# Kernel tuning notes

Hardware: AMD Instinct MI355X
Metric: run time of the kernel (lower is better)

Reference implementation:

```python
import jax, jax.numpy as jnp
import numpy as np

B, QL, CTX, H = 1, 2048, 2048, 4096
NH, NKV, HD = 32, 8, 128


def rotate_half(x):
    x1, x2 = jnp.split(x, 2, axis=-1)
    return jnp.concatenate([-x2, x1], axis=-1)


def apply_rotary(x, cos, sin):
    # x: [B, h, S, HD]; cos/sin: [B, S, HD] -> broadcast over heads
    cos = cos[:, None, :, :]
    sin = sin[:, None, :, :]
    return x * cos + rotate_half(x) * sin


def setup_inputs() -> dict:
    key = jax.random.key(0)
    ks = jax.random.split(key, 8)
    s = 0.02
    return {
        "hidden_states": jax.random.normal(ks[0], (B, QL, H), jnp.float32),
        "target_hidden": jax.random.normal(ks[1], (B, CTX, H), jnp.float32),
        "cos": jax.random.uniform(ks[2], (B, CTX + QL, HD), jnp.float32),
        "sin": jax.random.uniform(ks[3], (B, CTX + QL, HD), jnp.float32),
        "Wq": jax.random.normal(ks[4], (NH * HD, H), jnp.float32) * s,
        "Wk": jax.random.normal(ks[5], (NKV * HD, H), jnp.float32) * s,
        "Wv": jax.random.normal(ks[6], (NKV * HD, H), jnp.float32) * s,
        "Wo": jax.random.normal(ks[7], (H, NH * HD), jnp.float32) * s,
    }


def reference(hidden_states, target_hidden, cos, sin, Wq, Wk, Wv, Wo):
    bsz, q_len, _ = hidden_states.shape
    ctx_len = target_hidden.shape[1]

    def proj(x, W, nh):  # [B,S,H] @ W.T -> [B,nh,S,HD]
        y = jnp.einsum("bsh,dh->bsd", x, W)
        return y.reshape(bsz, x.shape[1], nh, HD).transpose(0, 2, 1, 3)

    q = proj(hidden_states, Wq, NH)
    k_ctx = proj(target_hidden, Wk, NKV)
    v_ctx = proj(target_hidden, Wv, NKV)
    k_noise = proj(hidden_states, Wk, NKV)
    v_noise = proj(hidden_states, Wv, NKV)

    cos_n = cos[:, ctx_len:ctx_len + q_len]
    sin_n = sin[:, ctx_len:ctx_len + q_len]
    q = apply_rotary(q, cos_n, sin_n)
    k_noise = apply_rotary(k_noise, cos_n, sin_n)
    k_ctx = apply_rotary(k_ctx, cos[:, :ctx_len], sin[:, :ctx_len])

    k = jnp.concatenate([k_ctx, k_noise], axis=2)  # [B,NKV,CTX+QL,HD]
    v = jnp.concatenate([v_ctx, v_noise], axis=2)

    n_rep = NH // NKV
    k = jnp.repeat(k, n_rep, axis=1)  # repeat_interleave on head dim
    v = jnp.repeat(v, n_rep, axis=1)

    scale = 1.0 / jnp.sqrt(jnp.asarray(HD, q.dtype))
    scores = jnp.einsum("bhqd,bhkd->bhqk", q, k) * scale
    probs = jax.nn.softmax(scores, axis=-1)
    attn = jnp.einsum("bhqk,bhkd->bhqd", probs, v)
    attn = attn.transpose(0, 2, 1, 3).reshape(bsz, q_len, NH * HD)
    return jnp.einsum("bsd,hd->bsh", attn, Wo)
```

## Files before the change

### kernel.cpp

```cpp
#include <hip/hip_runtime.h>

typedef unsigned short u16;
typedef _Float16 f16;
typedef _Float16 f16x4 __attribute__((ext_vector_type(4)));
typedef _Float16 f16x8 __attribute__((ext_vector_type(8)));
typedef float f32x4 __attribute__((ext_vector_type(4)));

#define GLL16(gptr, lptr)                                                        \
  __builtin_amdgcn_global_load_lds(                                              \
      (const __attribute__((address_space(1))) void*)(gptr),                     \
      (__attribute__((address_space(3))) void*)(lptr), 16, 0, 0)

__global__ void cast_all_k(const float* __restrict__ h, const float* __restrict__ t,
                           const float* __restrict__ wq, const float* __restrict__ wk,
                           const float* __restrict__ wv, const float* __restrict__ wo,
                           f16* __restrict__ Xcat, f16* __restrict__ Wqb,
                           f16* __restrict__ Wkvb, f16* __restrict__ Wob) {
  long i = (long)blockIdx.x * 256 + threadIdx.x;
  const float* s; f16* d; long off;
  if (i < 2097152)        { s = h;  d = Xcat;            off = i; }
  else if (i < 4194304)   { s = t;  d = Xcat + 8388608;  off = i - 2097152; }
  else if (i < 8388608)   { s = wq; d = Wqb;             off = i - 4194304; }
  else if (i < 9437184)   { s = wk; d = Wkvb;            off = i - 8388608; }
  else if (i < 10485760)  { s = wv; d = Wkvb + 4194304;  off = i - 9437184; }
  else                    { s = wo; d = Wob;             off = i - 10485760; }
  float4 v = *(const float4*)(s + off * 4);
  f16x4 o;
  o.x = (f16)v.x; o.y = (f16)v.y; o.z = (f16)v.z; o.w = (f16)v.w;
  *(f16x4*)(d + off * 4) = o;
}

template <int MODE>
__global__ __launch_bounds__(512, 2) void gemm8k(
    const f16* __restrict__ Xcat, const f16* __restrict__ Wqb,
    const f16* __restrict__ Wkvb, const float* __restrict__ cosT,
    const float* __restrict__ sinT, f16* __restrict__ Qb, f16* __restrict__ Kb,
    f16* __restrict__ Vt, const f16* __restrict__ Ao,
    const f16* __restrict__ Wob, float* __restrict__ Cp, float qscale) {
  __shared__ __align__(16) f16 lds[65536];
  const int tid = threadIdx.x;
  const int w = tid >> 6, lane = tid & 63;
  const int quad = lane >> 4, l16 = lane & 15;
  const int wm = w >> 1, wn = w & 1;

  int b = (int)blockIdx.x;
  int l = ((b & 7) << 5) | (b >> 3);

  const f16 *A, *B;
  long tM, tN;
  int NT, kbeg;
  bool isQ = false, isV = false;
  float* Cz = nullptr;
  if (MODE == 0) {
    kbeg = 0; NT = 64;
    if (l < 128) {
      A = Xcat; B = Wqb; tM = (long)(l >> 4) * 256; tN = (long)(l & 15) * 256;
      isQ = true;
    } else {
      int l2 = l - 128;
      A = Xcat; B = Wkvb; tM = (long)(l2 >> 3) * 256; tN = (long)(l2 & 7) * 256;
      isV = (tN >= 1024);
    }
  } else {
    int z = l >> 7, r0 = l & 127;
    A = Ao; B = Wob; tM = (long)(r0 >> 4) * 256; tN = (long)(r0 & 15) * 256;
    kbeg = z * 2048; NT = 32; Cz = Cp + (long)z * 8388608;
  }

  const int sr8 = lane >> 3;
  const int cg = (lane & 7) ^ sr8;
  const f16* Ag = A + (tM + 16 * w + sr8) * 4096 + kbeg + cg * 8;
  const f16* Bg = B + (tN + 16 * w + sr8) * 4096 + kbeg + cg * 8;
  const int ldsw = w * 1024;

#define STAGE_A(hf, t, c)                                                      \
  do {                                                                         \
    const f16* g_ = Ag + (long)(t) * 64 + (long)(hf) * (128 * 4096);           \
    f16* d_ = &lds[(c) * 16384 + (hf) * 8192 + ldsw];                          \
    GLL16(g_, d_);                                                             \
    GLL16(g_ + 8 * 4096, d_ + 512);                                            \
  } while (0)
#define STAGE_B(hf, t, c)                                                      \
  do {                                                                         \
    const f16* g_ = Bg + (long)(t) * 64 + (long)(hf) * (128 * 4096);           \
    f16* d_ = &lds[32768 + (c) * 16384 + (hf) * 8192 + ldsw];                  \
    GLL16(g_, d_);                                                             \
    GLL16(g_ + 8 * 4096, d_ + 512);                                            \
  } while (0)

  const int rA = wm * 64 + l16;
  const int rB = wn * 128 + l16;
  const int sw = l16 & 7;
#define LDA(fr, mi, kk, c)                                                     \
  fr = *(const f16x8*)&lds[(c) * 16384 + (rA + (mi) * 16) * 64 +               \
                           (((kk) * 4 + quad) ^ sw) * 8]
#define LDB(fr, ni, kk, c)                                                     \
  fr = *(const f16x8*)&lds[32768 + (c) * 16384 + (rB + (ni) * 16) * 64 +       \
                           (((kk) * 4 + quad) ^ sw) * 8]

#define MFMA16 __builtin_amdgcn_mfma_f32_16x16x32_f16
#define BAR() __builtin_amdgcn_s_barrier()
#define WAITDS()                                                               \
  do {                                                                         \
    asm volatile("s_waitcnt lgkmcnt(0)" ::: "memory");                         \
    __builtin_amdgcn_sched_barrier(0);                                         \
  } while (0)

  f32x4 acc[4][8] = {};
  f16x8 af[2][2], bf0[4][2], bf1[4][2];

  STAGE_B(0, 0, 0); STAGE_B(1, 0, 0); STAGE_A(0, 0, 0); STAGE_A(1, 0, 0);
  STAGE_B(0, 1, 1); STAGE_B(1, 1, 1);
  asm volatile("s_waitcnt vmcnt(4)" ::: "memory");
  BAR();

#define TILE_STEP(t, c)                                                        \
  do {                                                                         \
                                       \
    LDA(af[0][0], 0, 0, c); LDA(af[0][1], 0, 1, c);                            \
    LDA(af[1][0], 1, 0, c); LDA(af[1][1], 1, 1, c);                            \
    LDB(bf0[0][0], 0, 0, c); LDB(bf0[0][1], 0, 1, c);                          \
    LDB(bf0[1][0], 1, 0, c); LDB(bf0[1][1], 1, 1, c);                          \
    LDB(bf0[2][0], 2, 0, c); LDB(bf0[2][1], 2, 1, c);                          \
    LDB(bf0[3][0], 3, 0, c); LDB(bf0[3][1], 3, 1, c);                          \
    if ((t) + 1 < NT) STAGE_A(0, (t) + 1, (c) ^ 1);                            \
    BAR(); WAITDS();                                                           \
    __builtin_amdgcn_s_setprio(1);                                             \
    _Pragma("unroll") for (int mi = 0; mi < 2; ++mi)                           \
        _Pragma("unroll") for (int ni = 0; ni < 4; ++ni) {                     \
      acc[mi][ni] = MFMA16(af[mi][0], bf0[ni][0], acc[mi][ni], 0, 0, 0);       \
      acc[mi][ni] = MFMA16(af[mi][1], bf0[ni][1], acc[mi][ni], 0, 0, 0);       \
    }                                                                          \
    __builtin_amdgcn_s_setprio(0);                                             \
    BAR();                                                                     \
                                       \
    LDB(bf1[0][0], 4, 0, c); LDB(bf1[0][1], 4, 1, c);                          \
    LDB(bf1[1][0], 5, 0, c); LDB(bf1[1][1], 5, 1, c);                          \
    LDB(bf1[2][0], 6, 0, c); LDB(bf1[2][1], 6, 1, c);                          \
    LDB(bf1[3][0], 7, 0, c); LDB(bf1[3][1], 7, 1, c);                          \
    if ((t) + 1 < NT) STAGE_A(1, (t) + 1, (c) ^ 1);                            \
    BAR(); WAITDS();                                                           \
    __builtin_amdgcn_s_setprio(1);                                             \
    _Pragma("unroll") for (int mi = 0; mi < 2; ++mi)                           \
        _Pragma("unroll") for (int ni = 0; ni < 4; ++ni) {                     \
      acc[mi][4 + ni] =                                                        \
          MFMA16(af[mi][0], bf1[ni][0], acc[mi][4 + ni], 0, 0, 0);             \
      acc[mi][4 + ni] =                                                        \
          MFMA16(af[mi][1], bf1[ni][1], acc[mi][4 + ni], 0, 0, 0);             \
    }                                                                          \
    __builtin_amdgcn_s_setprio(0);                                             \
    BAR();                                                                     \
                                       \
    LDA(af[0][0], 2, 0, c); LDA(af[0][1], 2, 1, c);                            \
    LDA(af[1][0], 3, 0, c); LDA(af[1][1], 3, 1, c);                            \
    if ((t) + 2 < NT) STAGE_B(0, (t) + 2, c);                                  \
    BAR(); WAITDS();                                                           \
    __builtin_amdgcn_s_setprio(1);                                             \
    _Pragma("unroll") for (int mi = 0; mi < 2; ++mi)                           \
        _Pragma("unroll") for (int ni = 0; ni < 4; ++ni) {                     \
      acc[2 + mi][ni] = MFMA16(af[mi][0], bf0[ni][0], acc[2 + mi][ni], 0, 0, 0);\
      acc[2 + mi][ni] = MFMA16(af[mi][1], bf0[ni][1], acc[2 + mi][ni], 0, 0, 0);\
    }                                                                          \
    __builtin_amdgcn_s_setprio(0);                                             \
    BAR();                                                                     \
      \
    if ((t) + 2 < NT) STAGE_B(1, (t) + 2, c);                                  \
    BAR();                                                                     \
    __builtin_amdgcn_s_setprio(1);                                             \
    _Pragma("unroll") for (int mi = 0; mi < 2; ++mi)                           \
        _Pragma("unroll") for (int ni = 0; ni < 4; ++ni) {                     \
      acc[2 + mi][4 + ni] =                                                    \
          MFMA16(af[mi][0], bf1[ni][0], acc[2 + mi][4 + ni], 0, 0, 0);         \
      acc[2 + mi][4 + ni] =                                                    \
          MFMA16(af[mi][1], bf1[ni][1], acc[2 + mi][4 + ni], 0, 0, 0);         \
    }                                                                          \
    __builtin_amdgcn_s_setprio(0);                                             \
    if ((t) + 2 < NT)                                                          \
      asm volatile("s_waitcnt vmcnt(4)" ::: "memory");                         \
    else                                                                       \
      asm volatile("s_waitcnt vmcnt(0)" ::: "memory");                         \
    BAR();                                                                     \
  } while (0)

  for (int t = 0; t < NT; t += 2) {
    TILE_STEP(t, 0);
    TILE_STEP(t + 1, 1);
  }

  if (MODE == 1) {
#pragma unroll
    for (int mi = 0; mi < 4; ++mi)
#pragma unroll
      for (int ni = 0; ni < 8; ++ni)
#pragma unroll
        for (int r = 0; r < 4; ++r) {
          long row = tM + wm * 64 + mi * 16 + quad * 4 + r;
          long col = tN + wn * 128 + ni * 16 + l16;
          Cz[row * 4096 + col] = acc[mi][ni][r];
        }
  } else if (isV) {
    const int kvh = (int)((tN - 1024) >> 7) + wn;
#pragma unroll
    for (int mi = 0; mi < 4; ++mi) {
      int key0 = ((int)tM + wm * 64 + mi * 16 + quad * 4) ^ 2048;
#pragma unroll
      for (int ni = 0; ni < 8; ++ni) {
        int d = ni * 16 + l16;
        f16x4 pk;
#pragma unroll
        for (int r = 0; r < 4; ++r) pk[r] = (f16)acc[mi][ni][r];
        *(f16x4*)&Vt[((long)kvh * 128 + d) * 4096 + key0] = pk;
      }
    }
  } else {
    const float sc = isQ ? qscale : 1.0f;
    const int h = (int)(tN >> 7) + wn;
#pragma unroll
    for (int mi = 0; mi < 4; ++mi)
#pragma unroll
      for (int r = 0; r < 4; ++r) {
        int rg = (int)tM + wm * 64 + mi * 16 + quad * 4 + r;
        int pos = isQ ? (2048 + rg) : (rg ^ 2048);
        const float* cp = cosT + (long)pos * 128;
        const float* sp = sinT + (long)pos * 128;
        f16* orow = isQ ? Qb + ((long)h * 2048 + rg) * 128
                        : Kb + ((long)h * 4096 + pos) * 128;
#pragma unroll
        for (int ni = 0; ni < 4; ++ni) {
          int d = ni * 16 + l16;
          float x0 = acc[mi][ni][r], x1 = acc[mi][ni + 4][r];
          orow[d] = (f16)((x0 * cp[d] - x1 * sp[d]) * sc);
          orow[d + 64] = (f16)((x1 * cp[d + 64] + x0 * sp[d + 64]) * sc);
        }
      }
  }
#undef TILE_STEP
#undef STAGE_A
#undef STAGE_B
#undef LDA
#undef LDB
#undef WAITDS
#undef BAR
#undef MFMA16
}

__global__ __launch_bounds__(256, 2) void flash_k(const f16* __restrict__ Qb,
                                                  const f16* __restrict__ Kb,
                                                  const f16* __restrict__ Vt,
                                                  f16* __restrict__ Ob) {
  __shared__ __align__(16) f16 Ks[2][64 * 128];
  __shared__ __align__(16) f16 Vs[2][128 * 64];
  __shared__ __align__(16) f16 Ps[4][32 * 64];
  const int tid = threadIdx.x;
  const int w = tid >> 6, lane = tid & 63;
  const int quad = lane >> 4, l16 = lane & 15;
  const int b = blockIdx.x;
  const int kvh = b & 7;
  const int j = b >> 3;
  const int h = kvh * 4 + (j >> 4);
  const int q0 = (j & 15) * 128;

  f16x8 qf[2][4];
#pragma unroll
  for (int mi = 0; mi < 2; ++mi) {
    const f16* qrow = Qb + ((long)h * 2048 + q0 + w * 32 + mi * 16 + l16) * 128 + quad * 8;
#pragma unroll
    for (int kc = 0; kc < 4; ++kc) qf[mi][kc] = *(const f16x8*)(qrow + kc * 32);
  }

  f32x4 of[2][8] = {};
  float lsum[2] = {0.f, 0.f};
  const f16* Kg = Kb + (long)kvh * 4096 * 128;
  const f16* Vg = Vt + (long)kvh * 128 * 4096;
  f16* PsW = &Ps[w][0];
  const int psw = l16 & 7;

  const int krow = (lane >> 4);
  const int kslot = lane & 15;
  const int vrow = (lane >> 3);
  const int vslot = lane & 7;
  const int vgc = vslot ^ (vrow & 7);

#define FBAR() __builtin_amdgcn_s_barrier()
#define STAGE_K(kt_, c_)                                                       \
  do {                                                                         \
    _Pragma("unroll") for (int it = 0; it < 4; ++it) {                         \
      int row = w * 16 + it * 4 + krow;                                        \
      int gc = kslot ^ (it * 4 + krow);                                        \
      GLL16(Kg + (long)((kt_)*64 + row) * 128 + gc * 8,                        \
            &Ks[c_][(w * 16 + it * 4) * 128]);                                 \
    }                                                                          \
  } while (0)
#define STAGE_V(kt_, c_)                                                       \
  do {                                                                         \
    _Pragma("unroll") for (int it = 0; it < 4; ++it) {                         \
      int row = w * 32 + it * 8 + vrow;                                        \
      GLL16(Vg + (long)row * 4096 + (kt_)*64 + vgc * 8,                        \
            &Vs[c_][(w * 32 + it * 8) * 64]);                                  \
    }                                                                          \
  } while (0)

#define QKT(dst, c_)                                                           \
  do {                                                                         \
    _Pragma("unroll") for (int nt = 0; nt < 4; ++nt) {                         \
      f16x8 ak[4];                                                             \
      _Pragma("unroll") for (int kc = 0; kc < 4; ++kc) {                       \
        int slot = (kc * 4 + quad) ^ l16;                                      \
        ak[kc] = *(const f16x8*)&Ks[c_][(nt * 16 + l16) * 128 + slot * 8];     \
      }                                                                        \
      _Pragma("unroll") for (int mi = 0; mi < 2; ++mi)                         \
          _Pragma("unroll") for (int kc = 0; kc < 4; ++kc)                     \
        dst[mi][nt] = __builtin_amdgcn_mfma_f32_16x16x32_f16(                  \
            ak[kc], qf[mi][kc], dst[mi][nt], 0, 0, 0);                         \
    }                                                                          \
  } while (0)

#define EXPP(src)                                                              \
  do {                                                                         \
    _Pragma("unroll") for (int mi = 0; mi < 2; ++mi)                           \
        _Pragma("unroll") for (int nt = 0; nt < 4; ++nt) {                     \
      f16x4 pk;                                                                \
      _Pragma("unroll") for (int r = 0; r < 4; ++r) {                          \
        float pv = __builtin_amdgcn_exp2f(src[mi][nt][r]);                     \
        lsum[mi] += pv;                                                        \
        pk[r] = (f16)pv;                                                       \
      }                                                                        \
      *(f16x4*)&PsW[(mi * 16 + l16) * 64 +                                     \
                    (((nt * 2 + (quad >> 1)) ^ psw) << 3) + ((quad & 1) << 2)] \
          = pk;                                                                \
    }                                                                          \
  } while (0)

#define PVACC(vb_)                                                             \
  do {                                                                         \
    _Pragma("unroll") for (int kc2 = 0; kc2 < 2; ++kc2) {                      \
      f16x8 bp[2];                                                             \
      _Pragma("unroll") for (int mi = 0; mi < 2; ++mi)                         \
        bp[mi] = *(const f16x8*)&PsW[(mi * 16 + l16) * 64 +                    \
                                     (((kc2 * 4 + quad) ^ psw) << 3)];         \
      _Pragma("unroll") for (int dt = 0; dt < 8; ++dt) {                       \
        int slot = (kc2 * 4 + quad) ^ (l16 & 7);                               \
        f16x8 av = *(const f16x8*)&Vs[vb_][(dt * 16 + l16) * 64 + slot * 8];   \
        _Pragma("unroll") for (int mi = 0; mi < 2; ++mi)                       \
          of[mi][dt] = __builtin_amdgcn_mfma_f32_16x16x32_f16(                 \
              av, bp[mi], of[mi][dt], 0, 0, 0);                                \
      }                                                                        \
    }                                                                          \
  } while (0)

#define ZEROS(s_)                                                              \
  do {                                                                         \
    _Pragma("unroll") for (int mi = 0; mi < 2; ++mi)                           \
        _Pragma("unroll") for (int nt = 0; nt < 4; ++nt)                       \
            s_[mi][nt] = f32x4{0.f, 0.f, 0.f, 0.f};                            \
  } while (0)

#define ITER(kt_, c_, sPrev, sCur)                                             \
  do {                                                                         \
    asm volatile("s_waitcnt vmcnt(4)" ::: "memory");         \
    FBAR();                                                                    \
    __builtin_amdgcn_sched_barrier(0);                                         \
    ZEROS(sCur);                                                               \
    __builtin_amdgcn_s_setprio(1);                                             \
    QKT(sCur, c_);                                                             \
    EXPP(sPrev);                                                               \
    PVACC((c_) ^ 1);                                                           \
    __builtin_amdgcn_s_setprio(0);                                             \
    FBAR();                                                                    \
    if ((kt_) < 63) {                                                          \
      STAGE_K((kt_) + 1, (c_) ^ 1);                                            \
      STAGE_V((kt_) + 1, (c_) ^ 1);                                            \
    }                                                                          \
  } while (0)

  f32x4 sA[2][4], sB[2][4];

  STAGE_K(0, 0); STAGE_V(0, 0);
  STAGE_K(1, 1); STAGE_V(1, 1);
  asm volatile("s_waitcnt vmcnt(8)" ::: "memory");
  FBAR();
  __builtin_amdgcn_sched_barrier(0);
  ZEROS(sA);
  __builtin_amdgcn_s_setprio(1);
  QKT(sA, 0);
  __builtin_amdgcn_s_setprio(0);

  for (int kt = 1; kt < 63; kt += 2) {
    ITER(kt, 1, sA, sB);
    ITER(kt + 1, 0, sB, sA);
  }
  ITER(63, 1, sA, sB);

  EXPP(sB);
  asm volatile("s_waitcnt vmcnt(0)" ::: "memory");
  FBAR();
  PVACC(1);

#undef ITER
#undef ZEROS
#undef STAGE_K
#undef STAGE_V
#undef QKT
#undef EXPP
#undef PVACC
#undef FBAR

#pragma unroll
  for (int mi = 0; mi < 2; ++mi) {
    float v = lsum[mi];
    v += __shfl_xor(v, 16, 64);
    v += __shfl_xor(v, 32, 64);
    float inv = 1.0f / v;
    long q = q0 + w * 32 + mi * 16 + l16;
#pragma unroll
    for (int dt = 0; dt < 8; ++dt) {
      f16x4 o4;
#pragma unroll
      for (int r = 0; r < 4; ++r) o4[r] = (f16)(of[mi][dt][r] * inv);
      *(f16x4*)&Ob[q * 4096 + h * 128 + dt * 16 + quad * 4] = o4;
    }
  }
}

__global__ void reduce2_k(const float* __restrict__ p, float* __restrict__ out) {
  long i = ((long)blockIdx.x * 256 + threadIdx.x) * 4;
  float4 a = *(const float4*)(p + i);
  float4 b = *(const float4*)(p + 8388608 + i);
  a.x += b.x; a.y += b.y; a.z += b.z; a.w += b.w;
  *(float4*)(out + i) = a;
}

extern "C" void kernel_launch(void* const* d_in, const int* in_sizes, int n_in,
                              void* d_out, int out_size, void* d_ws, size_t ws_size,
                              hipStream_t stream) {
  (void)in_sizes; (void)n_in; (void)out_size; (void)ws_size;
  const float* hidden = (const float*)d_in[0];
  const float* target = (const float*)d_in[1];
  const float* cosT = (const float*)d_in[2];
  const float* sinT = (const float*)d_in[3];
  const float* Wq = (const float*)d_in[4];
  const float* Wk = (const float*)d_in[5];
  const float* Wv = (const float*)d_in[6];
  const float* Wo = (const float*)d_in[7];
  float* out = (float*)d_out;

  char* p = (char*)d_ws;
  auto alloc = [&](size_t bytes) {
    char* r = p;
    p += (bytes + 255) & ~(size_t)255;
    return r;
  };
  f16* Xcat = (f16*)alloc(4096ull * 4096 * 2);
  f16* Wqb  = (f16*)alloc(4096ull * 4096 * 2);
  f16* Wkvb = (f16*)alloc(2048ull * 4096 * 2);
  f16* Wob  = (f16*)alloc(4096ull * 4096 * 2);
  f16* Qb   = (f16*)alloc(32ull * 2048 * 128 * 2);
  f16* Kb   = (f16*)alloc(8ull * 4096 * 128 * 2);
  f16* Vt   = (f16*)alloc(8ull * 128 * 4096 * 2);
  f16* Ao   = (f16*)alloc(2048ull * 4096 * 2);
  float* Pp = (float*)d_ws;

  cast_all_k<<<57344, 256, 0, stream>>>(hidden, target, Wq, Wk, Wv, Wo,
                                        Xcat, Wqb, Wkvb, Wob);

  const float QSC = (float)(0.08838834764831845 * 1.4426950408889634);
  gemm8k<0><<<256, 512, 0, stream>>>(Xcat, Wqb, Wkvb, cosT, sinT, Qb, Kb, Vt,
                                     nullptr, nullptr, nullptr, QSC);

  flash_k<<<512, 256, 0, stream>>>(Qb, Kb, Vt, Ao);

  gemm8k<1><<<256, 512, 0, stream>>>(nullptr, nullptr, nullptr, nullptr, nullptr,
                                     nullptr, nullptr, nullptr, Ao, Wob, Pp, 0.f);
  reduce2_k<<<8192, 256, 0, stream>>>(Pp, out);
}
```

Baseline: 607.1 us.

## Split K and V staging into separate phases of the attention pipeline

Restructures the flash-attention inner loop so K and V tiles are prefetched at separate points. Each iteration now has two barrier phases: the first issues the next K tile and runs the PV accumulate, the second issues the V tile and runs QK^T and exp. The goal is to spread global-to-LDS traffic across the iteration and shorten waits on a combined K+V load. In exchange there are twice as many barriers per iteration and a longer hand-written prologue and epilogue that must keep the vmcnt counts and buffer indices correct.

```diff
diff --git a/kernel.cpp b/kernel.cpp
--- a/kernel.cpp
+++ b/kernel.cpp
@@ -282,6 +282,8 @@
   const int vgc = vslot ^ (vrow & 7);
 
 #define FBAR() __builtin_amdgcn_s_barrier()
+#define SCHED0() __builtin_amdgcn_sched_barrier(0)
+#define VMC(n) asm volatile("s_waitcnt vmcnt(" #n ")" ::: "memory")
 #define STAGE_K(kt_, c_)                                                       \
   do {                                                                         \
     _Pragma("unroll") for (int it = 0; it < 4; ++it) {                         \
@@ -355,46 +357,79 @@
             s_[mi][nt] = f32x4{0.f, 0.f, 0.f, 0.f};                            \
   } while (0)
 
-#define ITER(kt_, c_, sPrev, sCur)                                             \
-  do {                                                                         \
-    asm volatile("s_waitcnt vmcnt(4)" ::: "memory");         \
-    FBAR();                                                                    \
-    __builtin_amdgcn_sched_barrier(0);                                         \
-    ZEROS(sCur);                                                               \
+#define ITER(kt_, c_, sOld, sNew)                                              \
+  do {                                                                         \
+    VMC(8);                                           \
+    FBAR(); SCHED0();                                                          \
+    STAGE_K((kt_) + 1, (c_) ^ 1);                                              \
     __builtin_amdgcn_s_setprio(1);                                             \
-    QKT(sCur, c_);                                                             \
-    EXPP(sPrev);                                                               \
-    PVACC((c_) ^ 1);                                                           \
+    PVACC(c_);                                                   \
     __builtin_amdgcn_s_setprio(0);                                             \
-    FBAR();                                                                    \
-    if ((kt_) < 63) {                                                          \
-      STAGE_K((kt_) + 1, (c_) ^ 1);                                            \
-      STAGE_V((kt_) + 1, (c_) ^ 1);                                            \
-    }                                                                          \
+    VMC(8);                                             \
+    FBAR(); SCHED0();                                                          \
+    STAGE_V(kt_, c_);                                                          \
+    ZEROS(sNew);                                                               \
+    __builtin_amdgcn_s_setprio(1);                                             \
+    QKT(sNew, c_);                                                             \
+    EXPP(sOld);                                                                \
+    __builtin_amdgcn_s_setprio(0);                                             \
   } while (0)
 
   f32x4 sA[2][4], sB[2][4];
 
-  STAGE_K(0, 0); STAGE_V(0, 0);
-  STAGE_K(1, 1); STAGE_V(1, 1);
-  asm volatile("s_waitcnt vmcnt(8)" ::: "memory");
-  FBAR();
-  __builtin_amdgcn_sched_barrier(0);
+  STAGE_K(0, 0);
+  FBAR(); SCHED0();
+  STAGE_K(1, 1);
+  VMC(4);
+  FBAR(); SCHED0();
+  STAGE_V(0, 0);
   ZEROS(sA);
   __builtin_amdgcn_s_setprio(1);
   QKT(sA, 0);
   __builtin_amdgcn_s_setprio(0);
 
-  for (int kt = 1; kt < 63; kt += 2) {
-    ITER(kt, 1, sA, sB);
-    ITER(kt + 1, 0, sB, sA);
+  FBAR(); SCHED0();
+  STAGE_K(2, 0);
+  VMC(8);
+  FBAR(); SCHED0();
+  STAGE_V(1, 1);
+  ZEROS(sB);
+  __builtin_amdgcn_s_setprio(1);
+  QKT(sB, 1);
+  EXPP(sA);
+  __builtin_amdgcn_s_setprio(0);
+
+  for (int kt = 2; kt < 62; kt += 2) {
+    ITER(kt, 0, sB, sA);
+    ITER(kt + 1, 1, sA, sB);
   }
-  ITER(63, 1, sA, sB);
-
+  ITER(62, 0, sB, sA);
+
+  VMC(8);
+  FBAR(); SCHED0();
+  __builtin_amdgcn_s_setprio(1);
+  PVACC(1);
+  __builtin_amdgcn_s_setprio(0);
+  VMC(4);
+  FBAR(); SCHED0();
+  STAGE_V(63, 1);
+  ZEROS(sB);
+  __builtin_amdgcn_s_setprio(1);
+  QKT(sB, 1);
+  EXPP(sA);
+  __builtin_amdgcn_s_setprio(0);
+
+  VMC(4);
+  FBAR(); SCHED0();
+  __builtin_amdgcn_s_setprio(1);
+  PVACC(0);
+  __builtin_amdgcn_s_setprio(0);
   EXPP(sB);
-  asm volatile("s_waitcnt vmcnt(0)" ::: "memory");
-  FBAR();
+  VMC(0);
+  FBAR(); SCHED0();
+  __builtin_amdgcn_s_setprio(1);
   PVACC(1);
+  __builtin_amdgcn_s_setprio(0);
 
 #undef ITER
 #undef ZEROS
@@ -404,6 +439,8 @@
 #undef EXPP
 #undef PVACC
 #undef FBAR
+#undef SCHED0
+#undef VMC
 
 #pragma unroll
   for (int mi = 0; mi < 2; ++mi) {
```

New measurement: 624.9 us. 1.03x slower.
